# Optimization experiments

Measured on AMD Instinct MI355X. Metric: run time of the kernel, lower is better.

Reference implementation:

```python
import jax, jax.numpy as jnp
import numpy as np

N, E, G = 25000, 400000, 64
IN, HID, OUT = 16, 16, 16
EF, EH, NH, NC = 8, 64, 128, 10
EPS = 1e-5


def _seg_mean(vals, idx, n):
    s = jax.ops.segment_sum(vals, idx, num_segments=n)
    c = jax.ops.segment_sum(jnp.ones((idx.shape[0], 1), vals.dtype), idx, num_segments=n)
    return s / jnp.maximum(c, 1.0)


def _bn(x, g, b):
    m = x.mean(axis=0)
    v = x.var(axis=0)
    return (x - m) * jax.lax.rsqrt(v + EPS) * g + b


def _nnconv(x, src, dst, ew, root, bias, n_nodes, out_ch):
    # ew: [E, in*out] -> per-edge weight matrix [E, in, out]
    ew = ew.reshape(ew.shape[0], x.shape[1], out_ch)
    msg = jnp.einsum('ei,eio->eo', x[src], ew)  # gather + per-edge matmul
    agg = _seg_mean(msg, dst, n_nodes)          # scatter-mean at target nodes
    return x @ root + agg + bias


def setup_inputs():
    key = jax.random.key(0)
    ks = jax.random.split(key, 24)
    f = lambda k, shp, sc: jax.random.normal(k, shp, dtype=jnp.float32) * sc
    inp = {
        'x': f(ks[0], (N, IN), 1.0),
        'edge_src': jax.random.randint(ks[1], (E,), 0, N, dtype=jnp.int32),
        'edge_dst': jax.random.randint(ks[2], (E,), 0, N, dtype=jnp.int32),
        'edge_attr': f(ks[3], (E, EF), 1.0),
        'batch': jnp.sort(jax.random.randint(ks[4], (N,), 0, G, dtype=jnp.int32)),
        # edge MLP 1: Linear(EF,EH) -> ReLU -> Linear(EH, IN*HID)
        'en1_w1': f(ks[5], (EF, EH), 0.3), 'en1_b1': jnp.zeros((EH,), jnp.float32),
        'en1_w2': f(ks[6], (EH, IN * HID), 0.1), 'en1_b2': jnp.zeros((IN * HID,), jnp.float32),
        'root1': f(ks[7], (IN, HID), 0.25), 'bias1': jnp.zeros((HID,), jnp.float32),
        'bn1_g': jnp.ones((HID,), jnp.float32), 'bn1_b': jnp.zeros((HID,), jnp.float32),
        # edge net 2 (FC): single Linear(EF, HID*OUT)
        'en2_w': f(ks[8], (EF, HID * OUT), 0.1), 'en2_b': jnp.zeros((HID * OUT,), jnp.float32),
        'root2': f(ks[9], (HID, OUT), 0.25), 'bias2': jnp.zeros((OUT,), jnp.float32),
        'bn2_g': jnp.ones((OUT,), jnp.float32), 'bn2_b': jnp.zeros((OUT,), jnp.float32),
        'mlp_w1': f(ks[10], (OUT, NH), 0.25), 'mlp_b1': jnp.zeros((NH,), jnp.float32),
        'mlp_w2': f(ks[11], (NH, NC), 0.1), 'mlp_b2': jnp.zeros((NC,), jnp.float32),
    }
    return inp


def reference(x, edge_src, edge_dst, edge_attr, batch,
              en1_w1, en1_b1, en1_w2, en1_b2, root1, bias1, bn1_g, bn1_b,
              en2_w, en2_b, root2, bias2, bn2_g, bn2_b,
              mlp_w1, mlp_b1, mlp_w2, mlp_b2):
    # NNConv layer 1 (edge MLP -> per-edge weight -> gather-matmul-scatter-mean)
    ew1 = jax.nn.relu(edge_attr @ en1_w1 + en1_b1) @ en1_w2 + en1_b2
    h = _nnconv(x, edge_src, edge_dst, ew1, root1, bias1, N, HID)
    h = _bn(h, bn1_g, bn1_b)
    # NNConv layer 2 (single-Linear edge net)
    ew2 = edge_attr @ en2_w + en2_b
    h = _nnconv(h, edge_src, edge_dst, ew2, root2, bias2, N, OUT)
    h = _bn(h, bn2_g, bn2_b)
    # graph-level mean pooling
    g = _seg_mean(h, batch, G)
    # MLP head + log_softmax
    logits = jax.nn.relu(g @ mlp_w1 + mlp_b1) @ mlp_w2 + mlp_b2
    return jax.nn.log_softmax(logits, axis=1)
```

## Files before the change

### kernel.cpp

```cpp
#include <hip/hip_runtime.h>

#define NN 25000
#define NE 400000
#define NGR 64
#define NB3 391
#define K1B 1563
#define HISTB 512
#define EPS 1e-5f

static const size_t OFS_XWBUF  = 0;
static const size_t OFS_H1     = 0;
static const size_t OFS_XB2    = 12800000;
static const size_t OFS_MSG    = 13200000;
static const size_t OFS_STATS  = 19600000;
static const size_t OFS_EREC   = 19625600;
static const size_t OFS_OFF    = 26025600;
static const size_t OFS_CSCOFF = 26051200;
static const size_t OFS_OUTC   = 26076800;
static const size_t OFS_INC    = 26102400;
static const size_t OFS_BSUM   = 26128000;
static const size_t OFS_PART1  = 26128512;
static const size_t OFS_PART2  = 26141024;

__device__ __forceinline__ void atomAddF(float* p, float v) { unsafeAtomicAdd(p, v); }

__device__ __forceinline__ float4 add4(float4 a, float4 b) {
  float4 r; r.x=a.x+b.x; r.y=a.y+b.y; r.z=a.z+b.z; r.w=a.w+b.w; return r;
}
__device__ __forceinline__ void fma4(float4& p, float r, const float4 a) {
  p.x += r*a.x; p.y += r*a.y; p.z += r*a.z; p.w += r*a.w;
}
__device__ __forceinline__ unsigned short f2bf(float f) {
  unsigned u = __float_as_uint(f);
  u += 0x7FFFu + ((u >> 16) & 1u);
  return (unsigned short)(u >> 16);
}
__device__ __forceinline__ float bf2f(unsigned u16) {
  return __uint_as_float(u16 << 16);
}

__global__ __launch_bounds__(256) void k_hist_xw(const int* __restrict__ esrc,
    const int* __restrict__ edst, int* __restrict__ outc, int* __restrict__ inc,
    const float* __restrict__ x, const float* __restrict__ w2, const float* __restrict__ b2,
    unsigned short* __restrict__ xwbuf, float* __restrict__ xb2) {
  __shared__ float xs[16][17];
  if (blockIdx.x >= K1B) {
    const int base = (blockIdx.x - K1B)*256 + threadIdx.x;
    for (int e = base; e < NE; e += HISTB*256) {
      atomicAdd(&outc[esrc[e]], 1);
      atomicAdd(&inc[edst[e]], 1);
    }
    return;
  }
  const int t = threadIdx.x;
  const int h = t >> 2, og = (t & 3) * 4;
  const int nbase = blockIdx.x * 16;
  {
    const int n = nbase + (t >> 4), i = t & 15;
    xs[t >> 4][i] = (n < NN) ? x[(size_t)n*16 + i] : 0.f;
  }
  __syncthreads();
  float4 acc[16];
  #pragma unroll
  for (int n = 0; n < 16; ++n) acc[n] = make_float4(0.f,0.f,0.f,0.f);
  #pragma unroll
  for (int i = 0; i < 16; ++i) {
    const float4 w = *reinterpret_cast<const float4*>(&w2[h*256 + i*16 + og]);
    #pragma unroll
    for (int n = 0; n < 16; ++n) fma4(acc[n], xs[n][i], w);
  }
  #pragma unroll
  for (int n = 0; n < 16; ++n) {
    const int nn = nbase + n;
    if (nn < NN) {
      ushort4 s4;
      s4.x = f2bf(acc[n].x); s4.y = f2bf(acc[n].y);
      s4.z = f2bf(acc[n].z); s4.w = f2bf(acc[n].w);
      *reinterpret_cast<ushort4*>(&xwbuf[(size_t)nn*1024 + h*16 + og]) = s4;
    }
  }
  {
    const int n = nbase + (t >> 4), o = t & 15;
    if (n < NN) {
      float s = 0.f;
      #pragma unroll
      for (int i = 0; i < 16; ++i) s += xs[t >> 4][i] * b2[i*16 + o];
      xb2[(size_t)n*16 + o] = s;
    }
  }
}

__global__ __launch_bounds__(256) void k0_scanA(const int* __restrict__ outc,
    const int* __restrict__ inc, int* __restrict__ bsum) {
  __shared__ int rO[256], rI[256];
  const int t = threadIdx.x;
  const int i = blockIdx.x*256 + t;
  rO[t] = outc[i];
  rI[t] = inc[i];
  __syncthreads();
  for (int st = 128; st > 0; st >>= 1) {
    if (t < st) { rO[t] += rO[t+st]; rI[t] += rI[t+st]; }
    __syncthreads();
  }
  if (t == 0) { bsum[blockIdx.x] = rO[0]; bsum[100 + blockIdx.x] = rI[0]; }
}

__global__ __launch_bounds__(128) void k0_scanB(int* __restrict__ bsum) {
  __shared__ int sO[128], sI[128];
  const int t = threadIdx.x;
  const int cO = (t < 100) ? bsum[t] : 0;
  const int cI = (t < 100) ? bsum[100 + t] : 0;
  sO[t] = cO; sI[t] = cI;
  __syncthreads();
  for (int st = 1; st < 128; st <<= 1) {
    const int vO = (t >= st) ? sO[t-st] : 0;
    const int vI = (t >= st) ? sI[t-st] : 0;
    __syncthreads();
    sO[t] += vO; sI[t] += vI;
    __syncthreads();
  }
  if (t < 100) { bsum[200 + t] = sO[t] - cO; bsum[300 + t] = sI[t] - cI; }
}

__global__ __launch_bounds__(256) void k0_scanC(int* __restrict__ outc,
    int* __restrict__ inc, const int* __restrict__ bsum,
    int* __restrict__ off, int* __restrict__ cscoff) {
  __shared__ int sO[256], sI[256];
  const int t = threadIdx.x;
  const int i = blockIdx.x*256 + t;
  const int cO = outc[i];
  const int cI = inc[i];
  sO[t] = cO; sI[t] = cI;
  __syncthreads();
  for (int st = 1; st < 256; st <<= 1) {
    const int vO = (t >= st) ? sO[t-st] : 0;
    const int vI = (t >= st) ? sI[t-st] : 0;
    __syncthreads();
    sO[t] += vO; sI[t] += vI;
    __syncthreads();
  }
  if (i <= NN) {
    off[i]    = sO[t] - cO + bsum[200 + blockIdx.x];
    cscoff[i] = sI[t] - cI + bsum[300 + blockIdx.x];
  }
  outc[i] = 0;
  inc[i]  = 0;
}

__global__ __launch_bounds__(256) void k0_fill(const int* __restrict__ esrc,
    const int* __restrict__ edst, const float* __restrict__ ea,
    int* __restrict__ curs, int* __restrict__ curd,
    const int* __restrict__ off, const int* __restrict__ cscoff,
    float* __restrict__ erec) {
  for (int e = blockIdx.x*blockDim.x + threadIdx.x; e < NE; e += gridDim.x*blockDim.x) {
    const int s = esrc[e], d = edst[e];
    const float4 a = *reinterpret_cast<const float4*>(&ea[(size_t)e*8]);
    const float4 b = *reinterpret_cast<const float4*>(&ea[(size_t)e*8 + 4]);
    const int c1 = atomicAdd(&curs[s], 1);
    const int c2 = atomicAdd(&curd[d], 1);
    float* r = &erec[(size_t)(off[s] + c1)*16];
    *reinterpret_cast<float4*>(r)     = a;
    *reinterpret_cast<float4*>(r + 4) = b;
    *reinterpret_cast<int*>(r + 8)    = cscoff[d] + c2;
  }
}

__global__ __launch_bounds__(256) void k2_csr(const float* __restrict__ erec,
    const float* __restrict__ w1, const float* __restrict__ b1,
    const unsigned short* __restrict__ xwbuf, const float* __restrict__ xb2,
    const int* __restrict__ off, float* __restrict__ msg) {
  __shared__ float w1s[512];
  __shared__ float b1s[64];
  __shared__ float xwS[4][1024];
  __shared__ float rs[4][16][68];
  for (int idx = threadIdx.x; idx < 512; idx += 256) w1s[idx] = w1[idx];
  if (threadIdx.x < 64) b1s[threadIdx.x] = b1[threadIdx.x];
  __syncthreads();
  const int lane = threadIdx.x & 63, wl = threadIdx.x >> 6;
  const int el = lane >> 2, q = lane & 3;
  const int gw = blockIdx.x*4 + wl, nw = gridDim.x*4;
  float* xw = xwS[wl];
  float (*rsw)[68] = rs[wl];

  for (int n = gw; n < NN; n += nw) {
    const int st = off[n];
    const int deg = off[n+1] - st;
    if (deg == 0) continue;
    const uint4* src = reinterpret_cast<const uint4*>(&xwbuf[(size_t)n*1024]);
    #pragma unroll
    for (int j = 0; j < 2; ++j) {
      const uint4 v = src[j*64 + lane];
      const int base = (j*64 + lane)*8;
      float4 lo, hi;
      lo.x = bf2f(v.x & 0xFFFFu); lo.y = bf2f(v.x >> 16);
      lo.z = bf2f(v.y & 0xFFFFu); lo.w = bf2f(v.y >> 16);
      hi.x = bf2f(v.z & 0xFFFFu); hi.y = bf2f(v.z >> 16);
      hi.z = bf2f(v.w & 0xFFFFu); hi.w = bf2f(v.w >> 16);
      *reinterpret_cast<float4*>(&xw[base])     = lo;
      *reinterpret_cast<float4*>(&xw[base + 4]) = hi;
    }
    const float4 mb = *reinterpret_cast<const float4*>(&xb2[(size_t)n*16 + q*4]);
    __builtin_amdgcn_wave_barrier();

    for (int j0 = 0; j0 < deg; j0 += 16) {
      const int jj = j0 + el;
      const bool act = (jj < deg);
      const int slot = st + (act ? jj : 0);
      const float* rec = &erec[(size_t)slot*16];
      const float4 ea0 = *reinterpret_cast<const float4*>(rec);
      const float4 ea1 = *reinterpret_cast<const float4*>(rec + 4);
      const int pe = *reinterpret_cast<const int*>(rec + 8);
      const float eav[8] = {ea0.x, ea0.y, ea0.z, ea0.w, ea1.x, ea1.y, ea1.z, ea1.w};
      #pragma unroll
      for (int g = 0; g < 4; ++g) {
        float4 r4 = *reinterpret_cast<const float4*>(&b1s[q*16 + g*4]);
        #pragma unroll
        for (int f = 0; f < 8; ++f)
          fma4(r4, eav[f], *reinterpret_cast<const float4*>(&w1s[f*64 + q*16 + g*4]));
        r4.x = fmaxf(r4.x, 0.f); r4.y = fmaxf(r4.y, 0.f);
        r4.z = fmaxf(r4.z, 0.f); r4.w = fmaxf(r4.w, 0.f);
        *reinterpret_cast<float4*>(&rsw[el][q*16 + g*4]) = r4;
      }
      __builtin_amdgcn_wave_barrier();
      float4 m = mb;
      #pragma unroll
      for (int h0 = 0; h0 < 16; ++h0) {
        const float4 rv = *reinterpret_cast<const float4*>(&rsw[el][h0*4]);
        const float4 x0 = *reinterpret_cast<const float4*>(&xw[(h0*4+0)*16 + q*4]);
        const float4 x1 = *reinterpret_cast<const float4*>(&xw[(h0*4+1)*16 + q*4]);
        const float4 x2 = *reinterpret_cast<const float4*>(&xw[(h0*4+2)*16 + q*4]);
        const float4 x3 = *reinterpret_cast<const float4*>(&xw[(h0*4+3)*16 + q*4]);
        m.x += rv.x*x0.x + rv.y*x1.x + rv.z*x2.x + rv.w*x3.x;
        m.y += rv.x*x0.y + rv.y*x1.y + rv.z*x2.y + rv.w*x3.y;
        m.z += rv.x*x0.z + rv.y*x1.z + rv.z*x2.z + rv.w*x3.z;
        m.w += rv.x*x0.w + rv.y*x1.w + rv.z*x2.w + rv.w*x3.w;
      }
      if (act)
        *reinterpret_cast<float4*>(&msg[(size_t)pe*16 + q*4]) = m;
      __builtin_amdgcn_wave_barrier();
    }
  }
}

__global__ __launch_bounds__(256) void k3_node1(const float* __restrict__ x,
    const float* __restrict__ root1, const float* __restrict__ bias1,
    const float* __restrict__ msg, const int* __restrict__ cscoff,
    const float* __restrict__ bn_g, const float* __restrict__ bn_b,
    float* __restrict__ h1, float* __restrict__ part,
    float* __restrict__ stats, int* __restrict__ cnt) {
  __shared__ float rt[256];
  __shared__ float red[2][64][16];
  __shared__ float fr[8][33];
  __shared__ int isLast;
  rt[threadIdx.x] = root1[threadIdx.x];
  const int nl = threadIdx.x >> 2, qd = threadIdx.x & 3;
  const int n = blockIdx.x*64 + nl;
  float4 s1 = {0,0,0,0}, s2 = {0,0,0,0};
  __syncthreads();
  if (n < NN) {
    const int b0 = cscoff[n];
    const int deg = cscoff[n+1] - b0;
    float4 sm = {0,0,0,0};
    for (int j = 0; j < deg; ++j)
      sm = add4(sm, *reinterpret_cast<const float4*>(&msg[(size_t)(b0+j)*16 + qd*4]));
    float4 acc = *reinterpret_cast<const float4*>(&bias1[qd*4]);
    #pragma unroll
    for (int i = 0; i < 16; ++i)
      fma4(acc, x[(size_t)n*16 + i], *reinterpret_cast<const float4*>(&rt[i*16 + qd*4]));
    const float inv = 1.f / (float)((deg > 0) ? deg : 1);
    fma4(acc, inv, sm);
    *reinterpret_cast<float4*>(&h1[(size_t)n*16 + qd*4]) = acc;
    s1 = acc;
    s2.x = acc.x*acc.x; s2.y = acc.y*acc.y; s2.z = acc.z*acc.z; s2.w = acc.w*acc.w;
  }
  *reinterpret_cast<float4*>(&red[0][nl][qd*4]) = s1;
  *reinterpret_cast<float4*>(&red[1][nl][qd*4]) = s2;
  __syncthreads();
  for (int st = 32; st > 0; st >>= 1) {
    if (nl < st) {
      #pragma unroll
      for (int k = 0; k < 4; ++k) {
        red[0][nl][qd*4+k] += red[0][nl+st][qd*4+k];
        red[1][nl][qd*4+k] += red[1][nl+st][qd*4+k];
      }
    }
    __syncthreads();
  }
  if (nl == 0) {
    *reinterpret_cast<float4*>(&part[blockIdx.x*32 + qd*4]) =
        *reinterpret_cast<const float4*>(&red[0][0][qd*4]);
    *reinterpret_cast<float4*>(&part[blockIdx.x*32 + 16 + qd*4]) =
        *reinterpret_cast<const float4*>(&red[1][0][qd*4]);
  }
  __syncthreads();
  if (threadIdx.x == 0) {
    __threadfence();
    isLast = (atomicAdd(cnt, 1) == NB3 - 1);
  }
  __syncthreads();
  if (!isLast) return;
  __threadfence();
  {
    const int o = threadIdx.x & 31, c = threadIdx.x >> 5;
    float s = 0.f;
    for (int blk = c; blk < NB3; blk += 8) s += part[blk*32 + o];
    fr[c][o] = s;
    __syncthreads();
    if (threadIdx.x < 32) {
      float tot = fr[0][threadIdx.x];
      for (int k = 1; k < 8; ++k) tot += fr[k][threadIdx.x];
      fr[0][threadIdx.x] = tot;
    }
    __syncthreads();
    if (threadIdx.x < 16) {
      const int oo = threadIdx.x;
      const float mean = fr[0][oo] / (float)NN;
      const float var  = fr[0][16+oo] / (float)NN - mean*mean;
      const float sc   = bn_g[oo] * rsqrtf(var + EPS);
      stats[32+oo] = sc;
      stats[48+oo] = bn_b[oo] - mean*sc;
    }
  }
}

__global__ __launch_bounds__(256) void k6_csr(const float* __restrict__ erec,
    const float* __restrict__ h1, const float* __restrict__ stats,
    const float* __restrict__ w, const float* __restrict__ bvec,
    const int* __restrict__ off, float* __restrict__ msg) {
  __shared__ float ws2[2048];
  __shared__ float bs2[256];
  __shared__ float hwS[4][128];
  __shared__ float hbS[4][32];
  for (int idx = threadIdx.x; idx < 2048; idx += 256) ws2[idx] = w[idx];
  bs2[threadIdx.x] = bvec[threadIdx.x];
  __syncthreads();
  const int lane = threadIdx.x & 63, wl = threadIdx.x >> 6;
  const int el = lane >> 2, q = lane & 3;
  const int f = lane >> 3, o2 = (lane & 7) * 2;
  const int gw = blockIdx.x*4 + wl, nw = gridDim.x*4;
  for (int n = gw; n < NN; n += nw) {
    const int st = off[n];
    const int deg = off[n+1] - st;
    if (deg == 0) continue;
    if (lane < 16)
      hbS[wl][lane] = h1[(size_t)n*16 + lane]*stats[32+lane] + stats[48+lane];
    __builtin_amdgcn_wave_barrier();
    float a0 = 0.f, a1 = 0.f;
    #pragma unroll
    for (int i = 0; i < 16; ++i) {
      const float hv = hbS[wl][i];
      a0 += hv * ws2[f*256 + i*16 + o2];
      a1 += hv * ws2[f*256 + i*16 + o2 + 1];
    }
    hwS[wl][f*16 + o2] = a0; hwS[wl][f*16 + o2 + 1] = a1;
    if (lane < 16) {
      float s = 0.f;
      #pragma unroll
      for (int i = 0; i < 16; ++i) s += hbS[wl][i] * bs2[i*16 + lane];
      hbS[wl][16 + lane] = s;
    }
    __builtin_amdgcn_wave_barrier();
    const float4 mb = *reinterpret_cast<const float4*>(&hbS[wl][16 + q*4]);
    for (int j0 = 0; j0 < deg; j0 += 16) {
      const int jj = j0 + el;
      const bool act = (jj < deg);
      const int slot = st + (act ? jj : 0);
      const float* rec = &erec[(size_t)slot*16];
      const float4 ea0 = *reinterpret_cast<const float4*>(rec);
      const float4 ea1 = *reinterpret_cast<const float4*>(rec + 4);
      const int pe = *reinterpret_cast<const int*>(rec + 8);
      const float ef[8] = {ea0.x, ea0.y, ea0.z, ea0.w, ea1.x, ea1.y, ea1.z, ea1.w};
      float4 m = mb;
      #pragma unroll
      for (int ff = 0; ff < 8; ++ff)
        fma4(m, ef[ff], *reinterpret_cast<const float4*>(&hwS[wl][ff*16 + q*4]));
      if (act)
        *reinterpret_cast<float4*>(&msg[(size_t)pe*16 + q*4]) = m;
    }
    __builtin_amdgcn_wave_barrier();
  }
}

__global__ __launch_bounds__(256) void k7_node2(const float* __restrict__ h1,
    const float* __restrict__ root2, const float* __restrict__ bias2,
    const float* __restrict__ msg, const int* __restrict__ cscoff,
    const int* __restrict__ batch, const float* __restrict__ bn_g,
    const float* __restrict__ bn_b, float* __restrict__ stats,
    float* __restrict__ part, int* __restrict__ cnt) {
  __shared__ float rt[256];
  __shared__ float scs[16], shs[16];
  __shared__ float red[2][64][16];
  __shared__ float pool[64*17];
  __shared__ float fr[8][33];
  __shared__ int isLast;
  rt[threadIdx.x] = root2[threadIdx.x];
  if (threadIdx.x < 16) { scs[threadIdx.x] = stats[32+threadIdx.x]; shs[threadIdx.x] = stats[48+threadIdx.x]; }
  for (int idx = threadIdx.x; idx < 64*17; idx += 256) pool[idx] = 0.f;
  const int nl = threadIdx.x >> 2, qd = threadIdx.x & 3;
  const int n = blockIdx.x*64 + nl;
  float4 s1 = {0,0,0,0}, s2 = {0,0,0,0};
  __syncthreads();
  if (n < NN) {
    const int b0 = cscoff[n];
    const int deg = cscoff[n+1] - b0;
    float4 sm = {0,0,0,0};
    for (int j = 0; j < deg; ++j)
      sm = add4(sm, *reinterpret_cast<const float4*>(&msg[(size_t)(b0+j)*16 + qd*4]));
    float4 acc = *reinterpret_cast<const float4*>(&bias2[qd*4]);
    #pragma unroll
    for (int i = 0; i < 16; ++i) {
      const float hbn = h1[(size_t)n*16 + i]*scs[i] + shs[i];
      fma4(acc, hbn, *reinterpret_cast<const float4*>(&rt[i*16 + qd*4]));
    }
    const float inv = 1.f / (float)((deg > 0) ? deg : 1);
    fma4(acc, inv, sm);
    s1 = acc;
    s2.x = acc.x*acc.x; s2.y = acc.y*acc.y; s2.z = acc.z*acc.z; s2.w = acc.w*acc.w;
    const int g = batch[n];
    atomicAdd(&pool[g*17 + qd*4 + 0], acc.x);
    atomicAdd(&pool[g*17 + qd*4 + 1], acc.y);
    atomicAdd(&pool[g*17 + qd*4 + 2], acc.z);
    atomicAdd(&pool[g*17 + qd*4 + 3], acc.w);
    if (qd == 0) atomicAdd(&pool[g*17 + 16], 1.0f);
  }
  *reinterpret_cast<float4*>(&red[0][nl][qd*4]) = s1;
  *reinterpret_cast<float4*>(&red[1][nl][qd*4]) = s2;
  __syncthreads();
  for (int st = 32; st > 0; st >>= 1) {
    if (nl < st) {
      #pragma unroll
      for (int k = 0; k < 4; ++k) {
        red[0][nl][qd*4+k] += red[0][nl+st][qd*4+k];
        red[1][nl][qd*4+k] += red[1][nl+st][qd*4+k];
      }
    }
    __syncthreads();
  }
  if (nl == 0) {
    *reinterpret_cast<float4*>(&part[blockIdx.x*32 + qd*4]) =
        *reinterpret_cast<const float4*>(&red[0][0][qd*4]);
    *reinterpret_cast<float4*>(&part[blockIdx.x*32 + 16 + qd*4]) =
        *reinterpret_cast<const float4*>(&red[1][0][qd*4]);
  }
  for (int idx = threadIdx.x; idx < 64*17; idx += 256) {
    const float v = pool[idx];
    if (v != 0.f) {
      const int g = idx / 17, c = idx - g*17;
      atomAddF((c < 16) ? &stats[128 + g*16 + c] : &stats[1152 + g], v);
    }
  }
  __syncthreads();
  if (threadIdx.x == 0) {
    __threadfence();
    isLast = (atomicAdd(cnt, 1) == NB3 - 1);
  }
  __syncthreads();
  if (!isLast) return;
  __threadfence();
  {
    const int o = threadIdx.x & 31, c = threadIdx.x >> 5;
    float s = 0.f;
    for (int blk = c; blk < NB3; blk += 8) s += part[blk*32 + o];
    fr[c][o] = s;
    __syncthreads();
    if (threadIdx.x < 32) {
      float tot = fr[0][threadIdx.x];
      for (int k = 1; k < 8; ++k) tot += fr[k][threadIdx.x];
      fr[0][threadIdx.x] = tot;
    }
    __syncthreads();
    if (threadIdx.x < 16) {
      const int oo = threadIdx.x;
      const float mean = fr[0][oo] / (float)NN;
      const float var  = fr[0][16+oo] / (float)NN - mean*mean;
      const float sc   = bn_g[oo] * rsqrtf(var + EPS);
      stats[96+oo]  = sc;
      stats[112+oo] = bn_b[oo] - mean*sc;
    }
  }
}

__global__ __launch_bounds__(128) void k10_head(const float* __restrict__ stats,
    const float* __restrict__ w1, const float* __restrict__ b1,
    const float* __restrict__ w2, const float* __restrict__ b2,
    float* __restrict__ out) {
  __shared__ float gm[16];
  __shared__ float a[128];
  __shared__ float l[10];
  __shared__ float mls[2];
  const int g = blockIdx.x, j = threadIdx.x;
  if (j < 16) {
    const float cnt = fmaxf(stats[1152 + g], 1.0f);
    gm[j] = (stats[128 + g*16 + j] / cnt) * stats[96 + j] + stats[112 + j];
  }
  __syncthreads();
  float s = b1[j];
  #pragma unroll
  for (int o = 0; o < 16; ++o) s += gm[o]*w1[o*128 + j];
  a[j] = fmaxf(s, 0.f);
  __syncthreads();
  if (j < 10) {
    float t = b2[j];
    #pragma unroll 16
    for (int k = 0; k < 128; ++k) t += a[k]*w2[k*10 + j];
    l[j] = t;
  }
  __syncthreads();
  if (j == 0) {
    float m = l[0];
    for (int c = 1; c < 10; ++c) m = fmaxf(m, l[c]);
    float se = 0.f;
    for (int c = 0; c < 10; ++c) se += expf(l[c]-m);
    mls[0] = m; mls[1] = logf(se);
  }
  __syncthreads();
  if (j < 10) out[g*10 + j] = l[j] - mls[0] - mls[1];
}

extern "C" void kernel_launch(void* const* d_in, const int* in_sizes, int n_in,
                              void* d_out, int out_size, void* d_ws, size_t ws_size,
                              hipStream_t stream) {
  const float* x      = (const float*)d_in[0];
  const int*   esrc   = (const int*)  d_in[1];
  const int*   edst   = (const int*)  d_in[2];
  const float* ea     = (const float*)d_in[3];
  const int*   batch  = (const int*)  d_in[4];
  const float* en1_w1 = (const float*)d_in[5];
  const float* en1_b1 = (const float*)d_in[6];
  const float* en1_w2 = (const float*)d_in[7];
  const float* en1_b2 = (const float*)d_in[8];
  const float* root1  = (const float*)d_in[9];
  const float* bias1  = (const float*)d_in[10];
  const float* bn1_g  = (const float*)d_in[11];
  const float* bn1_b  = (const float*)d_in[12];
  const float* en2_w  = (const float*)d_in[13];
  const float* en2_b  = (const float*)d_in[14];
  const float* root2  = (const float*)d_in[15];
  const float* bias2  = (const float*)d_in[16];
  const float* bn2_g  = (const float*)d_in[17];
  const float* bn2_b  = (const float*)d_in[18];
  const float* mlp_w1 = (const float*)d_in[19];
  const float* mlp_b1 = (const float*)d_in[20];
  const float* mlp_w2 = (const float*)d_in[21];
  const float* mlp_b2 = (const float*)d_in[22];
  float* out = (float*)d_out;
  float* ws  = (float*)d_ws;

  unsigned short* xwbuf = (unsigned short*)(ws + OFS_XWBUF);
  float* xb2    = ws + OFS_XB2;
  float* msg    = ws + OFS_MSG;
  float* stats  = ws + OFS_STATS;
  float* erec   = ws + OFS_EREC;
  float* h1     = ws + OFS_H1;
  float* part1  = ws + OFS_PART1;
  float* part2  = ws + OFS_PART2;
  int*   off    = (int*)(ws + OFS_OFF);
  int*   cscoff = (int*)(ws + OFS_CSCOFF);
  int*   outc   = (int*)(ws + OFS_OUTC);
  int*   inc    = (int*)(ws + OFS_INC);
  int*   bsum   = (int*)(ws + OFS_BSUM);
  int*   cnt1   = (int*)(stats + 1216);
  int*   cnt2   = (int*)(stats + 1217);

  hipMemsetAsync(outc,  0, 51200*sizeof(int), stream);
  hipMemsetAsync(stats, 0, 2048*sizeof(float), stream);

  hipLaunchKernelGGL(k_hist_xw, dim3(K1B + HISTB), dim3(256), 0, stream,
                     esrc, edst, outc, inc, x, en1_w2, en1_b2, xwbuf, xb2);
  hipLaunchKernelGGL(k0_scanA, dim3(100), dim3(256), 0, stream, outc, inc, bsum);
  hipLaunchKernelGGL(k0_scanB, dim3(1),   dim3(128), 0, stream, bsum);
  hipLaunchKernelGGL(k0_scanC, dim3(100), dim3(256), 0, stream, outc, inc, bsum, off, cscoff);
  hipLaunchKernelGGL(k0_fill,  dim3(1024),dim3(256), 0, stream, esrc, edst, ea, outc, inc,
                     off, cscoff, erec);

  hipLaunchKernelGGL(k2_csr,   dim3(1024), dim3(256), 0, stream, erec, en1_w1, en1_b1,
                     xwbuf, xb2, off, msg);
  hipLaunchKernelGGL(k3_node1, dim3(NB3),  dim3(256), 0, stream, x, root1, bias1, msg, cscoff,
                     bn1_g, bn1_b, h1, part1, stats, cnt1);

  hipLaunchKernelGGL(k6_csr,   dim3(1024), dim3(256), 0, stream, erec, h1, stats,
                     en2_w, en2_b, off, msg);
  hipLaunchKernelGGL(k7_node2, dim3(NB3),  dim3(256), 0, stream, h1, root2, bias2, msg, cscoff,
                     batch, bn2_g, bn2_b, stats, part2, cnt2);

  hipLaunchKernelGGL(k10_head, dim3(64), dim3(128), 0, stream, stats, mlp_w1, mlp_b1, mlp_w2, mlp_b2, out);
}
```

Baseline: 259.7 us.

## Compute per-edge NNConv layer-1 messages with bf16 MFMA instead of scalar FMAs

```diff
diff --git a/kernel.cpp b/kernel.cpp
--- a/kernel.cpp
+++ b/kernel.cpp
@@ -21,6 +21,9 @@
 static const size_t OFS_BSUM   = 26128000;
 static const size_t OFS_PART1  = 26128512;
 static const size_t OFS_PART2  = 26141024;
+
+typedef __attribute__((ext_vector_type(8))) short v8s;
+typedef __attribute__((ext_vector_type(4))) float v4f;
 
 __device__ __forceinline__ void atomAddF(float* p, float v) { unsafeAtomicAdd(p, v); }
 
@@ -171,73 +174,70 @@
     const int* __restrict__ off, float* __restrict__ msg) {
   __shared__ float w1s[512];
   __shared__ float b1s[64];
-  __shared__ float xwS[4][1024];
-  __shared__ float rs[4][16][68];
   for (int idx = threadIdx.x; idx < 512; idx += 256) w1s[idx] = w1[idx];
   if (threadIdx.x < 64) b1s[threadIdx.x] = b1[threadIdx.x];
   __syncthreads();
   const int lane = threadIdx.x & 63, wl = threadIdx.x >> 6;
-  const int el = lane >> 2, q = lane & 3;
+  const int eidx = lane & 15;
+  const int kg   = lane >> 4;
+  const int hb0  = kg*8;
+  const int hb1  = 32 + kg*8;
   const int gw = blockIdx.x*4 + wl, nw = gridDim.x*4;
-  float* xw = xwS[wl];
-  float (*rsw)[68] = rs[wl];
 
   for (int n = gw; n < NN; n += nw) {
     const int st = off[n];
     const int deg = off[n+1] - st;
     if (deg == 0) continue;
-    const uint4* src = reinterpret_cast<const uint4*>(&xwbuf[(size_t)n*1024]);
+    const unsigned short* xwn = &xwbuf[(size_t)n*1024];
+    v8s bf0, bf1;
     #pragma unroll
-    for (int j = 0; j < 2; ++j) {
-      const uint4 v = src[j*64 + lane];
-      const int base = (j*64 + lane)*8;
-      float4 lo, hi;
-      lo.x = bf2f(v.x & 0xFFFFu); lo.y = bf2f(v.x >> 16);
-      lo.z = bf2f(v.y & 0xFFFFu); lo.w = bf2f(v.y >> 16);
-      hi.x = bf2f(v.z & 0xFFFFu); hi.y = bf2f(v.z >> 16);
-      hi.z = bf2f(v.w & 0xFFFFu); hi.w = bf2f(v.w >> 16);
-      *reinterpret_cast<float4*>(&xw[base])     = lo;
-      *reinterpret_cast<float4*>(&xw[base + 4]) = hi;
-    }
-    const float4 mb = *reinterpret_cast<const float4*>(&xb2[(size_t)n*16 + q*4]);
-    __builtin_amdgcn_wave_barrier();
+    for (int j = 0; j < 8; ++j) {
+      bf0[j] = (short)xwn[(hb0 + j)*16 + eidx];
+      bf1[j] = (short)xwn[(hb1 + j)*16 + eidx];
+    }
+    const float xbv = xb2[(size_t)n*16 + eidx];
 
     for (int j0 = 0; j0 < deg; j0 += 16) {
-      const int jj = j0 + el;
-      const bool act = (jj < deg);
-      const int slot = st + (act ? jj : 0);
+      const int jj = j0 + eidx;
+      const int slot = st + ((jj < deg) ? jj : (deg - 1));
       const float* rec = &erec[(size_t)slot*16];
       const float4 ea0 = *reinterpret_cast<const float4*>(rec);
       const float4 ea1 = *reinterpret_cast<const float4*>(rec + 4);
       const int pe = *reinterpret_cast<const int*>(rec + 8);
       const float eav[8] = {ea0.x, ea0.y, ea0.z, ea0.w, ea1.x, ea1.y, ea1.z, ea1.w};
-      #pragma unroll
-      for (int g = 0; g < 4; ++g) {
-        float4 r4 = *reinterpret_cast<const float4*>(&b1s[q*16 + g*4]);
-        #pragma unroll
-        for (int f = 0; f < 8; ++f)
-          fma4(r4, eav[f], *reinterpret_cast<const float4*>(&w1s[f*64 + q*16 + g*4]));
-        r4.x = fmaxf(r4.x, 0.f); r4.y = fmaxf(r4.y, 0.f);
-        r4.z = fmaxf(r4.z, 0.f); r4.w = fmaxf(r4.w, 0.f);
-        *reinterpret_cast<float4*>(&rsw[el][q*16 + g*4]) = r4;
+      float4 rA0 = *reinterpret_cast<const float4*>(&b1s[hb0]);
+      float4 rA1 = *reinterpret_cast<const float4*>(&b1s[hb0 + 4]);
+      float4 rB0 = *reinterpret_cast<const float4*>(&b1s[hb1]);
+      float4 rB1 = *reinterpret_cast<const float4*>(&b1s[hb1 + 4]);
+      #pragma unroll
+      for (int f = 0; f < 8; ++f) {
+        const float ef = eav[f];
+        fma4(rA0, ef, *reinterpret_cast<const float4*>(&w1s[f*64 + hb0]));
+        fma4(rA1, ef, *reinterpret_cast<const float4*>(&w1s[f*64 + hb0 + 4]));
+        fma4(rB0, ef, *reinterpret_cast<const float4*>(&w1s[f*64 + hb1]));
+        fma4(rB1, ef, *reinterpret_cast<const float4*>(&w1s[f*64 + hb1 + 4]));
       }
-      __builtin_amdgcn_wave_barrier();
-      float4 m = mb;
-      #pragma unroll
-      for (int h0 = 0; h0 < 16; ++h0) {
-        const float4 rv = *reinterpret_cast<const float4*>(&rsw[el][h0*4]);
-        const float4 x0 = *reinterpret_cast<const float4*>(&xw[(h0*4+0)*16 + q*4]);
-        const float4 x1 = *reinterpret_cast<const float4*>(&xw[(h0*4+1)*16 + q*4]);
-        const float4 x2 = *reinterpret_cast<const float4*>(&xw[(h0*4+2)*16 + q*4]);
-        const float4 x3 = *reinterpret_cast<const float4*>(&xw[(h0*4+3)*16 + q*4]);
-        m.x += rv.x*x0.x + rv.y*x1.x + rv.z*x2.x + rv.w*x3.x;
-        m.y += rv.x*x0.y + rv.y*x1.y + rv.z*x2.y + rv.w*x3.y;
-        m.z += rv.x*x0.z + rv.y*x1.z + rv.z*x2.z + rv.w*x3.z;
-        m.w += rv.x*x0.w + rv.y*x1.w + rv.z*x2.w + rv.w*x3.w;
+      v8s af0, af1;
+      af0[0] = (short)f2bf(fmaxf(rA0.x, 0.f)); af0[1] = (short)f2bf(fmaxf(rA0.y, 0.f));
+      af0[2] = (short)f2bf(fmaxf(rA0.z, 0.f)); af0[3] = (short)f2bf(fmaxf(rA0.w, 0.f));
+      af0[4] = (short)f2bf(fmaxf(rA1.x, 0.f)); af0[5] = (short)f2bf(fmaxf(rA1.y, 0.f));
+      af0[6] = (short)f2bf(fmaxf(rA1.z, 0.f)); af0[7] = (short)f2bf(fmaxf(rA1.w, 0.f));
+      af1[0] = (short)f2bf(fmaxf(rB0.x, 0.f)); af1[1] = (short)f2bf(fmaxf(rB0.y, 0.f));
+      af1[2] = (short)f2bf(fmaxf(rB0.z, 0.f)); af1[3] = (short)f2bf(fmaxf(rB0.w, 0.f));
+      af1[4] = (short)f2bf(fmaxf(rB1.x, 0.f)); af1[5] = (short)f2bf(fmaxf(rB1.y, 0.f));
+      af1[6] = (short)f2bf(fmaxf(rB1.z, 0.f)); af1[7] = (short)f2bf(fmaxf(rB1.w, 0.f));
+
+      v4f acc = {0.f, 0.f, 0.f, 0.f};
+      acc = __builtin_amdgcn_mfma_f32_16x16x32_bf16(af0, bf0, acc, 0, 0, 0);
+      acc = __builtin_amdgcn_mfma_f32_16x16x32_bf16(af1, bf1, acc, 0, 0, 0);
+
+      #pragma unroll
+      for (int r = 0; r < 4; ++r) {
+        const int er = kg*4 + r;
+        const int pr = __shfl(pe, er);
+        if (j0 + er < deg)
+          msg[(size_t)pr*16 + eidx] = acc[r] + xbv;
       }
-      if (act)
-        *reinterpret_cast<float4*>(&msg[(size_t)pe*16 + q*4]) = m;
-      __builtin_amdgcn_wave_barrier();
     }
   }
 }
```

New measurement: 239.8 us. 1.08x faster.
